# Kernel optimization log

Measured on AMD Instinct MI355X. Metric: run time of the kernel, lower is better.

The kernel has to match this reference:

```python
import jax, jax.numpy as jnp
import numpy as np

F8_MAX = 448.0   # max representable magnitude of float8_e4m3fn
EPS = 1e-12      # amax clamp from the source


def setup_inputs() -> dict:
    key = jax.random.key(0)
    kx, kw, kb = jax.random.split(key, 3)
    B, S, K, N = 8, 8192, 1024, 1024
    x = jax.random.normal(kx, (B, S, K), dtype=jnp.float32)
    weight = jax.random.normal(kw, (N, K), dtype=jnp.float32) * 0.02  # (out, in) like nn.Linear
    bias = jax.random.normal(kb, (N,), dtype=jnp.float32)
    return {"x": x, "weight": weight, "bias": bias}


def _quantize_fp8(t):
    """Per-tensor dynamic fp8-e4m3 quantization: returns (t_fp8, scale)."""
    scale = jnp.maximum(jnp.max(jnp.abs(t)), EPS) / F8_MAX
    t8 = (t / scale).astype(jnp.float8_e4m3fn)
    return t8, scale


def reference(x, weight, bias):
    lead = x.shape[:-1]
    K = x.shape[-1]
    N = weight.shape[0]
    x_flat = x.reshape(-1, K).astype(jnp.float32)

    # dynamic activation quantization (forward-time, per tensor)
    x8, x_scale = _quantize_fp8(x_flat)
    # weight quantization (from_linear, per tensor)
    w8, w_scale = _quantize_fp8(weight.astype(jnp.float32))

    out = jnp.dot(x8.astype(jnp.float32), w8.astype(jnp.float32).T) * (x_scale * w_scale)
    out = out.astype(x.dtype).reshape(*lead, N)
    return out + bias
```

## Files before the change

### kernel.cpp

```cpp
#include <hip/hip_runtime.h>
#include <stdint.h>

#define F8MAX 448.0f
#define QEPS 1e-12f
#define SCL_ONE 0x7F7F7F7F
#define AXB 4096

typedef float floatx16 __attribute__((ext_vector_type(16)));
typedef int   intx4    __attribute__((ext_vector_type(4)));
typedef int   intx8    __attribute__((ext_vector_type(8)));

__global__ __launch_bounds__(256) void amax_partial_xw(
    const float* __restrict__ x, int nx4,
    const float* __restrict__ w, int nw4,
    float* __restrict__ px, float* __restrict__ pw)
{
    const float4* x4 = (const float4*)x;
    const float4* w4 = (const float4*)w;
    int tid = blockIdx.x * 256 + threadIdx.x;
    int stride = gridDim.x * 256;
    float mx = 0.f, mw = 0.f;
    for (int i = tid; i < nx4; i += stride) {
        float4 v = x4[i];
        mx = fmaxf(mx, fmaxf(fmaxf(fabsf(v.x), fabsf(v.y)), fmaxf(fabsf(v.z), fabsf(v.w))));
    }
    for (int i = tid; i < nw4; i += stride) {
        float4 v = w4[i];
        mw = fmaxf(mw, fmaxf(fmaxf(fabsf(v.x), fabsf(v.y)), fmaxf(fabsf(v.z), fabsf(v.w))));
    }
    #pragma unroll
    for (int off = 32; off > 0; off >>= 1) {
        mx = fmaxf(mx, __shfl_xor(mx, off, 64));
        mw = fmaxf(mw, __shfl_xor(mw, off, 64));
    }
    __shared__ float smx[4], smw[4];
    if ((threadIdx.x & 63) == 0) { smx[threadIdx.x >> 6] = mx; smw[threadIdx.x >> 6] = mw; }
    __syncthreads();
    if (threadIdx.x == 0) {
        px[blockIdx.x] = fmaxf(fmaxf(smx[0], smx[1]), fmaxf(smx[2], smx[3]));
        pw[blockIdx.x] = fmaxf(fmaxf(smw[0], smw[1]), fmaxf(smw[2], smw[3]));
    }
}

__global__ __launch_bounds__(512) void quant_fused(
    const float* __restrict__ x, const float* __restrict__ w,
    uint8_t* __restrict__ x8, uint8_t* __restrict__ w8,
    const float* __restrict__ px, const float* __restrict__ pw,
    unsigned* __restrict__ hdr, int nhx, int nkt, int K)
{
    __shared__ uint8_t lds[32768];

    int bid = blockIdx.x;
    bool isw = (bid < 32);
    const float* par = isw ? pw : px;

    float m = 0.f;
    for (int i = threadIdx.x; i < AXB; i += 512) m = fmaxf(m, par[i]);
    #pragma unroll
    for (int off = 32; off > 0; off >>= 1) m = fmaxf(m, __shfl_xor(m, off, 64));
    __shared__ float red[8];
    if ((threadIdx.x & 63) == 0) red[threadIdx.x >> 6] = m;
    __syncthreads();
    float amax = red[0];
    #pragma unroll
    for (int i = 1; i < 8; i++) amax = fmaxf(amax, red[i]);

    float scale = fmaxf(amax, QEPS) / F8MAX;
    float rs = 1.0f / scale;

    if (threadIdx.x == 0) {
        if (bid == 0)  hdr[1] = __float_as_uint(amax);
        if (bid == 32) hdr[0] = __float_as_uint(amax);
    }

    int hp = isw ? bid : (nhx - 1 - (bid - 32));
    const float* src = isw ? w : x;
    uint8_t* dst8 = isw ? w8 : x8;
    int p = hp >> 2, q = hp & 3;

    int wave = threadIdx.x >> 6, lane = threadIdx.x & 63;
    int K4 = K >> 2;

    const float4* s4 = (const float4*)src + (size_t)hp * 32 * K4;
    uint32_t key = (lane >> 2) & 7;
    uint32_t lbase = ((uint32_t)(lane >> 4) * 2048) + (((lane >> 2) & 3) * 512) + ((lane & 3) * 4);
    #pragma unroll
    for (int rr = 0; rr < 4; rr++) {
        int r = rr * 8 + wave;
        const float4* rowp = s4 + (size_t)r * K4;
        #pragma unroll
        for (int j = 0; j < 4; j++) {
            float4 f = rowp[j * 64 + lane];
            int wd = 0;
            wd = __builtin_amdgcn_cvt_pk_fp8_f32(f.x * rs, f.y * rs, wd, false);
            wd = __builtin_amdgcn_cvt_pk_fp8_f32(f.z * rs, f.w * rs, wd, true);
            uint32_t a = (uint32_t)j * 8192 + lbase + (uint32_t)r * 16;
            a ^= (key << 4);
            *(int*)(lds + a) = wd;
        }
    }
    __syncthreads();

    uint8_t* outb = dst8 + (size_t)(p * nkt) * 8192 + q * 512;
    int l32 = lane & 31, chi = lane >> 5;
    #pragma unroll
    for (int it = 0; it < 4; it++) {
        int c = it * 16 + wave * 2 + chi;
        int kt = c >> 2, hpc = c & 3;
        uint32_t k2 = (uint32_t)(((kt & 1) << 2) | hpc);
        uint32_t a = (uint32_t)c * 512 + (((uint32_t)l32 * 16) ^ (k2 << 4));
        int4 v = *(const int4*)(lds + a);
        *(int4*)(outb + (size_t)kt * 8192 + hpc * 2048 + l32 * 16) = v;
    }
}

__global__ __launch_bounds__(512, 1) void gemm_fp8_mx(
    const uint8_t* __restrict__ A8, const uint8_t* __restrict__ B8,
    float* __restrict__ C, const float* __restrict__ bias,
    const unsigned* __restrict__ hdr, int N, int nkt, int nbn)
{
    __shared__ uint8_t lsA[4 * 16384];
    __shared__ uint8_t lsB[4 * 16384];

    int nwg = gridDim.x;
    int bid = blockIdx.x;
    if ((nwg & 7) == 0) {
        int chunk = nwg >> 3;
        bid = (blockIdx.x & 7) * chunk + (blockIdx.x >> 3);
    }
    int bm = bid / nbn, bn = bid - bm * nbn;

    int t = threadIdx.x;
    int wave = t >> 6, lane = t & 63;
    int wr = wave >> 2, wc = wave & 3;
    int hl = lane >> 5, l31 = lane & 31;

    const uint8_t* gsrc0; const uint8_t* gsrc1; const uint8_t* gsrc2; const uint8_t* gsrc3;
    uint32_t ld0, ld1, ld2, ld3;
    bool isA = (wave < 4);
    {
        int c0 = wave * 4;
        #pragma unroll
        for (int p = 0; p < 4; p++) {
            int c = c0 + p;
            const uint8_t* g;
            uint32_t l;
            if (c < 16) {
                int h = c >> 3, sub = c & 7;
                g = A8 + (size_t)(bm * 2 + h) * nkt * 8192 + sub * 1024 + lane * 16;
                l = (uint32_t)c * 1024;
            } else {
                int cc = c - 16, h = cc >> 3, sub = cc & 7;
                g = B8 + (size_t)(bn * 2 + h) * nkt * 8192 + sub * 1024 + lane * 16;
                l = (uint32_t)cc * 1024;
            }
            if (p == 0) { gsrc0 = g; ld0 = l; }
            else if (p == 1) { gsrc1 = g; ld1 = l; }
            else if (p == 2) { gsrc2 = g; ld2 = l; }
            else { gsrc3 = g; ld3 = l; }
        }
    }
    uint8_t* lsbase = isA ? lsA : lsB;

#define ISSUE(GP, LO, KT2, B2)                                                   \
    __builtin_amdgcn_global_load_lds(                                            \
        (const __attribute__((address_space(1))) void*)((GP) + (size_t)(KT2) * 8192), \
        (__attribute__((address_space(3))) void*)(lsbase + (B2) * 16384 + (LO)), \
        16, 0, 0)

    const uint8_t* baseA = lsA + wr * 8192 + hl * 4096 + l31 * 16;
    const uint8_t* baseB = lsB + (wc >> 1) * 8192 + hl * 4096 + (wc & 1) * 1024 + l31 * 16;

    floatx16 acc[4][2];
    #pragma unroll
    for (int m = 0; m < 4; m++)
        #pragma unroll
        for (int n = 0; n < 2; n++)
            acc[m][n] = (floatx16)(0.0f);

#define RD8(BASE, OFF) __builtin_shufflevector(                         \
        *(const intx4*)((BASE) + (OFF)),                                \
        *(const intx4*)((BASE) + (OFF) + 2048), 0, 1, 2, 3, 4, 5, 6, 7)

#define MMX(m, n) acc[m][n] = __builtin_amdgcn_mfma_scale_f32_32x32x64_f8f6f4( \
        af[m], bf[n], acc[m][n], 0, 0, 0, SCL_ONE, 0, SCL_ONE)

    ISSUE(gsrc0, ld0, 0, 0); ISSUE(gsrc1, ld1, 0, 0); ISSUE(gsrc2, ld2, 0, 0); ISSUE(gsrc3, ld3, 0, 0);
    ISSUE(gsrc0, ld0, 1, 1); ISSUE(gsrc1, ld1, 1, 1); ISSUE(gsrc2, ld2, 1, 1); ISSUE(gsrc3, ld3, 1, 1);
    ISSUE(gsrc0, ld0, 2, 2); ISSUE(gsrc1, ld1, 2, 2); ISSUE(gsrc2, ld2, 2, 2); ISSUE(gsrc3, ld3, 2, 2);
    asm volatile("s_waitcnt vmcnt(8)" ::: "memory");
    asm volatile("s_barrier" ::: "memory");

    for (int kt = 0; kt < nkt; kt++) {
        int cur = kt & 3;
        int ib = (cur + 3) & 3;
        const uint8_t* cA = baseA + cur * 16384;
        const uint8_t* cB = baseB + cur * 16384;
        intx8 af[4], bf[2];

        if (kt + 3 < nkt) {
            ISSUE(gsrc0, ld0, kt + 3, ib); ISSUE(gsrc1, ld1, kt + 3, ib);
            ISSUE(gsrc2, ld2, kt + 3, ib); ISSUE(gsrc3, ld3, kt + 3, ib);
        }

        af[0] = RD8(cA, 0);    af[1] = RD8(cA, 512);
        bf[0] = RD8(cB, 0);    bf[1] = RD8(cB, 512);
        af[2] = RD8(cA, 1024); af[3] = RD8(cA, 1536);

        __builtin_amdgcn_s_setprio(1);
        MMX(0, 0); MMX(0, 1); MMX(1, 0); MMX(1, 1);
        MMX(2, 0); MMX(2, 1); MMX(3, 0); MMX(3, 1);
        __builtin_amdgcn_s_setprio(0);

        if (kt + 1 < nkt) {
            if (kt + 4 <= nkt - 1)      asm volatile("s_waitcnt vmcnt(8)" ::: "memory");
            else if (kt + 3 <= nkt - 1) asm volatile("s_waitcnt vmcnt(4)" ::: "memory");
            else                        asm volatile("s_waitcnt vmcnt(0)" ::: "memory");
            asm volatile("s_barrier" ::: "memory");
        }
    }

    float sxv = fmaxf(__uint_as_float(hdr[0]), QEPS) / F8MAX;
    float swv = fmaxf(__uint_as_float(hdr[1]), QEPS) / F8MAX;
    float s = sxv * swv;

    #pragma unroll
    for (int m = 0; m < 4; m++) {
        int row0 = bm * 256 + wr * 128 + m * 32 + 4 * hl;
        #pragma unroll
        for (int n = 0; n < 2; n++) {
            int col = bn * 256 + wc * 64 + n * 32 + l31;
            float bv = bias[col];
            #pragma unroll
            for (int reg = 0; reg < 16; reg++) {
                int row = row0 + (reg & 3) + 8 * (reg >> 2);
                __builtin_nontemporal_store(acc[m][n][reg] * s + bv, &C[(size_t)row * N + col]);
            }
        }
    }
#undef ISSUE
#undef RD8
#undef MMX
}

extern "C" void kernel_launch(void* const* d_in, const int* in_sizes, int n_in,
                              void* d_out, int out_size, void* d_ws, size_t ws_size,
                              hipStream_t stream)
{
    const float* x    = (const float*)d_in[0];
    const float* w    = (const float*)d_in[1];
    const float* bias = (const float*)d_in[2];
    float* out = (float*)d_out;

    int N = in_sizes[2];
    int K = in_sizes[1] / N;
    int M = in_sizes[0] / K;
    int nx = in_sizes[0];
    int nw = in_sizes[1];
    int nkt = K / 64;

    uint8_t* ws = (uint8_t*)d_ws;
    unsigned* hdr = (unsigned*)ws;
    float* px = (float*)(ws + 64);
    float* pw = (float*)(ws + 64 + 16384);
    uint8_t* w8 = ws + 65536;
    uint8_t* x8 = ws + 65536 + (size_t)N * K;

    int nhx = M / 32;
    int nhw = N / 32;

    amax_partial_xw<<<AXB, 256, 0, stream>>>(x, nx / 4, w, nw / 4, px, pw);
    quant_fused<<<nhw + nhx, 512, 0, stream>>>(x, w, x8, w8, px, pw, hdr, nhx, nkt, K);

    int nbm = M / 256, nbn = N / 256;
    gemm_fp8_mx<<<nbm * nbn, 512, 0, stream>>>(x8, w8, out, bias, hdr, N, nkt, nbn);
}
```

Before: 203.8 us.

## Fuse activation fp8 quantization into GEMM mainloop, quantize only weights separately

The separate pass that quantized x to fp8 in global memory is removed. The GEMM now loads fp32 x tiles straight into registers, converts them to fp8 with the global scale, and writes them swizzled into LDS. The buffering drops from 4 to 2 stages, and each iteration waits for all loads with vmcnt(0). This saves writing and re-reading the fp8 copy of x, but every GEMM block along N (4 blocks here) re-reads the fp32 x tile at four times the byte size, and the shallower pipeline exposes more load latency.

```diff
diff --git a/kernel.cpp b/kernel.cpp
--- a/kernel.cpp
+++ b/kernel.cpp
@@ -42,20 +42,14 @@
     }
 }
 
-__global__ __launch_bounds__(512) void quant_fused(
-    const float* __restrict__ x, const float* __restrict__ w,
-    uint8_t* __restrict__ x8, uint8_t* __restrict__ w8,
-    const float* __restrict__ px, const float* __restrict__ pw,
-    unsigned* __restrict__ hdr, int nhx, int nkt, int K)
+__global__ __launch_bounds__(512) void quant_w(
+    const float* __restrict__ w, uint8_t* __restrict__ w8,
+    const float* __restrict__ pw, int nkt, int K)
 {
     __shared__ uint8_t lds[32768];
 
-    int bid = blockIdx.x;
-    bool isw = (bid < 32);
-    const float* par = isw ? pw : px;
-
     float m = 0.f;
-    for (int i = threadIdx.x; i < AXB; i += 512) m = fmaxf(m, par[i]);
+    for (int i = threadIdx.x; i < AXB; i += 512) m = fmaxf(m, pw[i]);
     #pragma unroll
     for (int off = 32; off > 0; off >>= 1) m = fmaxf(m, __shfl_xor(m, off, 64));
     __shared__ float red[8];
@@ -68,20 +62,12 @@
     float scale = fmaxf(amax, QEPS) / F8MAX;
     float rs = 1.0f / scale;
 
-    if (threadIdx.x == 0) {
-        if (bid == 0)  hdr[1] = __float_as_uint(amax);
-        if (bid == 32) hdr[0] = __float_as_uint(amax);
-    }
-
-    int hp = isw ? bid : (nhx - 1 - (bid - 32));
-    const float* src = isw ? w : x;
-    uint8_t* dst8 = isw ? w8 : x8;
+    int hp = blockIdx.x;
     int p = hp >> 2, q = hp & 3;
-
     int wave = threadIdx.x >> 6, lane = threadIdx.x & 63;
     int K4 = K >> 2;
 
-    const float4* s4 = (const float4*)src + (size_t)hp * 32 * K4;
+    const float4* s4 = (const float4*)w + (size_t)hp * 32 * K4;
     uint32_t key = (lane >> 2) & 7;
     uint32_t lbase = ((uint32_t)(lane >> 4) * 2048) + (((lane >> 2) & 3) * 512) + ((lane & 3) * 4);
     #pragma unroll
@@ -101,7 +87,7 @@
     }
     __syncthreads();
 
-    uint8_t* outb = dst8 + (size_t)(p * nkt) * 8192 + q * 512;
+    uint8_t* outb = w8 + (size_t)(p * nkt) * 8192 + q * 512;
     int l32 = lane & 31, chi = lane >> 5;
     #pragma unroll
     for (int it = 0; it < 4; it++) {
@@ -114,13 +100,39 @@
     }
 }
 
-__global__ __launch_bounds__(512, 1) void gemm_fp8_mx(
-    const uint8_t* __restrict__ A8, const uint8_t* __restrict__ B8,
+__global__ __launch_bounds__(512, 1) void gemm_fused(
+    const float* __restrict__ x, const uint8_t* __restrict__ B8,
     float* __restrict__ C, const float* __restrict__ bias,
-    const unsigned* __restrict__ hdr, int N, int nkt, int nbn)
-{
-    __shared__ uint8_t lsA[4 * 16384];
-    __shared__ uint8_t lsB[4 * 16384];
+    const float* __restrict__ px, const float* __restrict__ pw,
+    int N, int K, int nkt, int nbn, int nbm)
+{
+    __shared__ uint8_t lsA[2 * 16384];
+    __shared__ uint8_t lsB[2 * 16384];
+
+    int wave = threadIdx.x >> 6, lane = threadIdx.x & 63;
+    int wr = wave >> 2, wc = wave & 3;
+    int hl = lane >> 5, l31 = lane & 31;
+
+    float m1 = 0.f, m2 = 0.f;
+    for (int i = threadIdx.x; i < AXB; i += 512) {
+        m1 = fmaxf(m1, px[i]);
+        m2 = fmaxf(m2, pw[i]);
+    }
+    #pragma unroll
+    for (int off = 32; off > 0; off >>= 1) {
+        m1 = fmaxf(m1, __shfl_xor(m1, off, 64));
+        m2 = fmaxf(m2, __shfl_xor(m2, off, 64));
+    }
+    __shared__ float redx[8], redw[8];
+    if (lane == 0) { redx[wave] = m1; redw[wave] = m2; }
+    __syncthreads();
+    float ax = redx[0], aw = redw[0];
+    #pragma unroll
+    for (int i = 1; i < 8; i++) { ax = fmaxf(ax, redx[i]); aw = fmaxf(aw, redw[i]); }
+    float sclx = fmaxf(ax, QEPS) / F8MAX;
+    float sclw = fmaxf(aw, QEPS) / F8MAX;
+    float rsx = 1.0f / sclx;
+    float s = sclx * sclw;
 
     int nwg = gridDim.x;
     int bid = blockIdx.x;
@@ -129,47 +141,25 @@
         bid = (blockIdx.x & 7) * chunk + (blockIdx.x >> 3);
     }
     int bm = bid / nbn, bn = bid - bm * nbn;
-
-    int t = threadIdx.x;
-    int wave = t >> 6, lane = t & 63;
-    int wr = wave >> 2, wc = wave & 3;
-    int hl = lane >> 5, l31 = lane & 31;
-
-    const uint8_t* gsrc0; const uint8_t* gsrc1; const uint8_t* gsrc2; const uint8_t* gsrc3;
-    uint32_t ld0, ld1, ld2, ld3;
-    bool isA = (wave < 4);
-    {
-        int c0 = wave * 4;
-        #pragma unroll
-        for (int p = 0; p < 4; p++) {
-            int c = c0 + p;
-            const uint8_t* g;
-            uint32_t l;
-            if (c < 16) {
-                int h = c >> 3, sub = c & 7;
-                g = A8 + (size_t)(bm * 2 + h) * nkt * 8192 + sub * 1024 + lane * 16;
-                l = (uint32_t)c * 1024;
-            } else {
-                int cc = c - 16, h = cc >> 3, sub = cc & 7;
-                g = B8 + (size_t)(bn * 2 + h) * nkt * 8192 + sub * 1024 + lane * 16;
-                l = (uint32_t)cc * 1024;
-            }
-            if (p == 0) { gsrc0 = g; ld0 = l; }
-            else if (p == 1) { gsrc1 = g; ld1 = l; }
-            else if (p == 2) { gsrc2 = g; ld2 = l; }
-            else { gsrc3 = g; ld3 = l; }
-        }
-    }
-    uint8_t* lsbase = isA ? lsA : lsB;
-
-#define ISSUE(GP, LO, KT2, B2)                                                   \
-    __builtin_amdgcn_global_load_lds(                                            \
-        (const __attribute__((address_space(1))) void*)((GP) + (size_t)(KT2) * 8192), \
-        (__attribute__((address_space(3))) void*)(lsbase + (B2) * 16384 + (LO)), \
-        16, 0, 0)
-
-    const uint8_t* baseA = lsA + wr * 8192 + hl * 4096 + l31 * 16;
-    const uint8_t* baseB = lsB + (wc >> 1) * 8192 + hl * 4096 + (wc & 1) * 1024 + l31 * 16;
+    bm = nbm - 1 - bm;
+
+    const float* gx = x + (size_t)(bm * 256 + (threadIdx.x >> 4)) * K + (threadIdx.x & 15) * 4;
+
+    uint32_t awbase = (((threadIdx.x >> 3) & 1) * 4096) + (((threadIdx.x >> 2) & 1) * 2048)
+                    + ((threadIdx.x & 3) * 4);
+    uint32_t wkey = (((uint32_t)threadIdx.x >> 2) & 3) << 4;
+    int r_lo = threadIdx.x >> 4;
+
+    int c0 = wave * 2, c1 = wave * 2 + 1;
+    const uint8_t* gB0 = B8 + (size_t)(bn * 2 + (c0 >> 3)) * nkt * 8192 + (c0 & 7) * 1024 + lane * 16;
+    const uint8_t* gB1 = B8 + (size_t)(bn * 2 + (c1 >> 3)) * nkt * 8192 + (c1 & 7) * 1024 + lane * 16;
+    uint32_t lb0 = (uint32_t)c0 * 1024, lb1 = (uint32_t)c1 * 1024;
+
+    uint32_t aR = (uint32_t)wr * 8192 + (uint32_t)hl * 4096 + (uint32_t)l31 * 16;
+    uint32_t keyA0 = (uint32_t)(hl * 2 + 0) << 4;
+    uint32_t keyA1 = (uint32_t)(hl * 2 + 1) << 4;
+    uint32_t bR = (uint32_t)(wc >> 1) * 8192 + (uint32_t)hl * 4096 + (uint32_t)(wc & 1) * 1024
+                + (uint32_t)l31 * 16;
 
     floatx16 acc[4][2];
     #pragma unroll
@@ -178,51 +168,84 @@
         for (int n = 0; n < 2; n++)
             acc[m][n] = (floatx16)(0.0f);
 
-#define RD8(BASE, OFF) __builtin_shufflevector(                         \
-        *(const intx4*)((BASE) + (OFF)),                                \
-        *(const intx4*)((BASE) + (OFF) + 2048), 0, 1, 2, 3, 4, 5, 6, 7)
-
-#define MMX(m, n) acc[m][n] = __builtin_amdgcn_mfma_scale_f32_32x32x64_f8f6f4( \
+#define LOADA(KT, F)                                                              \
+    {                                                                             \
+        const float* ga = gx + (size_t)(KT) * 64;                                 \
+        _Pragma("unroll")                                                         \
+        for (int k = 0; k < 8; k++)                                               \
+            F[k] = *(const float4*)(ga + (size_t)k * 32 * K);                     \
+    }
+
+#define LOADB(KT, BO)                                                             \
+    __builtin_amdgcn_global_load_lds(                                             \
+        (const __attribute__((address_space(1))) void*)(gB0 + (size_t)(KT) * 8192), \
+        (__attribute__((address_space(3))) void*)(lsB + (BO) + lb0), 16, 0, 0);   \
+    __builtin_amdgcn_global_load_lds(                                             \
+        (const __attribute__((address_space(1))) void*)(gB1 + (size_t)(KT) * 8192), \
+        (__attribute__((address_space(3))) void*)(lsB + (BO) + lb1), 16, 0, 0)
+
+#define CVTWRITE(F, BO)                                                           \
+    {                                                                             \
+        _Pragma("unroll")                                                         \
+        for (int k = 0; k < 8; k++) {                                             \
+            int wd = 0;                                                           \
+            wd = __builtin_amdgcn_cvt_pk_fp8_f32(F[k].x * rsx, F[k].y * rsx, wd, false); \
+            wd = __builtin_amdgcn_cvt_pk_fp8_f32(F[k].z * rsx, F[k].w * rsx, wd, true);  \
+            int r = k * 32 + r_lo;                                                \
+            uint32_t a = (((uint32_t)(r >> 7) * 8192 + (uint32_t)(r & 127) * 16 + awbase) ^ wkey); \
+            *(int*)(lsA + (BO) + a) = wd;                                         \
+        }                                                                         \
+    }
+
+#define RDA(M, BO) __builtin_shufflevector(                                        \
+        *(const intx4*)(lsA + (BO) + ((aR + (M) * 512) ^ keyA0)),                  \
+        *(const intx4*)(lsA + (BO) + ((aR + (M) * 512 + 2048) ^ keyA1)),           \
+        0, 1, 2, 3, 4, 5, 6, 7)
+
+#define RDB(Nn, BO) __builtin_shufflevector(                                       \
+        *(const intx4*)(lsB + (BO) + (bR + (Nn) * 512)),                           \
+        *(const intx4*)(lsB + (BO) + (bR + (Nn) * 512 + 2048)),                    \
+        0, 1, 2, 3, 4, 5, 6, 7)
+
+#define MMX(m, n) acc[m][n] = __builtin_amdgcn_mfma_scale_f32_32x32x64_f8f6f4(     \
         af[m], bf[n], acc[m][n], 0, 0, 0, SCL_ONE, 0, SCL_ONE)
 
-    ISSUE(gsrc0, ld0, 0, 0); ISSUE(gsrc1, ld1, 0, 0); ISSUE(gsrc2, ld2, 0, 0); ISSUE(gsrc3, ld3, 0, 0);
-    ISSUE(gsrc0, ld0, 1, 1); ISSUE(gsrc1, ld1, 1, 1); ISSUE(gsrc2, ld2, 1, 1); ISSUE(gsrc3, ld3, 1, 1);
-    ISSUE(gsrc0, ld0, 2, 2); ISSUE(gsrc1, ld1, 2, 2); ISSUE(gsrc2, ld2, 2, 2); ISSUE(gsrc3, ld3, 2, 2);
-    asm volatile("s_waitcnt vmcnt(8)" ::: "memory");
-    asm volatile("s_barrier" ::: "memory");
+    {
+        float4 f0[8];
+        LOADA(0, f0);
+        LOADB(0, 0);
+        asm volatile("s_waitcnt vmcnt(0)" ::: "memory");
+        CVTWRITE(f0, 0);
+    }
+    __syncthreads();
 
     for (int kt = 0; kt < nkt; kt++) {
-        int cur = kt & 3;
-        int ib = (cur + 3) & 3;
-        const uint8_t* cA = baseA + cur * 16384;
-        const uint8_t* cB = baseB + cur * 16384;
+        uint32_t bo = (uint32_t)(kt & 1) * 16384;
+        uint32_t bo2 = bo ^ 16384;
+        bool pf = (kt + 1 < nkt);
+        float4 f[8];
+
+        if (pf) {
+            LOADA(kt + 1, f);
+            LOADB(kt + 1, bo2);
+        }
+
         intx8 af[4], bf[2];
-
-        if (kt + 3 < nkt) {
-            ISSUE(gsrc0, ld0, kt + 3, ib); ISSUE(gsrc1, ld1, kt + 3, ib);
-            ISSUE(gsrc2, ld2, kt + 3, ib); ISSUE(gsrc3, ld3, kt + 3, ib);
-        }
-
-        af[0] = RD8(cA, 0);    af[1] = RD8(cA, 512);
-        bf[0] = RD8(cB, 0);    bf[1] = RD8(cB, 512);
-        af[2] = RD8(cA, 1024); af[3] = RD8(cA, 1536);
+        af[0] = RDA(0, bo); af[1] = RDA(1, bo);
+        bf[0] = RDB(0, bo); bf[1] = RDB(1, bo);
+        af[2] = RDA(2, bo); af[3] = RDA(3, bo);
 
         __builtin_amdgcn_s_setprio(1);
         MMX(0, 0); MMX(0, 1); MMX(1, 0); MMX(1, 1);
         MMX(2, 0); MMX(2, 1); MMX(3, 0); MMX(3, 1);
         __builtin_amdgcn_s_setprio(0);
 
-        if (kt + 1 < nkt) {
-            if (kt + 4 <= nkt - 1)      asm volatile("s_waitcnt vmcnt(8)" ::: "memory");
-            else if (kt + 3 <= nkt - 1) asm volatile("s_waitcnt vmcnt(4)" ::: "memory");
-            else                        asm volatile("s_waitcnt vmcnt(0)" ::: "memory");
-            asm volatile("s_barrier" ::: "memory");
-        }
-    }
-
-    float sxv = fmaxf(__uint_as_float(hdr[0]), QEPS) / F8MAX;
-    float swv = fmaxf(__uint_as_float(hdr[1]), QEPS) / F8MAX;
-    float s = sxv * swv;
+        if (pf) {
+            asm volatile("s_waitcnt vmcnt(0)" ::: "memory");
+            CVTWRITE(f, bo2);
+        }
+        __syncthreads();
+    }
 
     #pragma unroll
     for (int m = 0; m < 4; m++) {
@@ -238,8 +261,11 @@
             }
         }
     }
-#undef ISSUE
-#undef RD8
+#undef LOADA
+#undef LOADB
+#undef CVTWRITE
+#undef RDA
+#undef RDB
 #undef MMX
 }
 
@@ -260,18 +286,13 @@
     int nkt = K / 64;
 
     uint8_t* ws = (uint8_t*)d_ws;
-    unsigned* hdr = (unsigned*)ws;
     float* px = (float*)(ws + 64);
     float* pw = (float*)(ws + 64 + 16384);
     uint8_t* w8 = ws + 65536;
-    uint8_t* x8 = ws + 65536 + (size_t)N * K;
-
-    int nhx = M / 32;
-    int nhw = N / 32;
 
     amax_partial_xw<<<AXB, 256, 0, stream>>>(x, nx / 4, w, nw / 4, px, pw);
-    quant_fused<<<nhw + nhx, 512, 0, stream>>>(x, w, x8, w8, px, pw, hdr, nhx, nkt, K);
+    quant_w<<<N / 32, 512, 0, stream>>>(w, w8, pw, nkt, K);
 
     int nbm = M / 256, nbn = N / 256;
-    gemm_fp8_mx<<<nbm * nbn, 512, 0, stream>>>(x8, w8, out, bias, hdr, N, nkt, nbn);
-}
+    gemm_fused<<<nbm * nbn, 512, 0, stream>>>(x, w8, out, bias, px, pw, N, K, nkt, nbn, nbm);
+}
```

Measured after the change: 224.5 us. 1.1x slower.
